# Kernel optimization log

Hardware: AMD Instinct MI355X
Metric: run time of the kernel (lower is better)

## Reference

```python
import jax, jax.numpy as jnp
import numpy as np

B, N, T, D, H, L, N_HOP = 8, 512, 64, 256, 256, 2, 1
NEG = -1e18


def setup_inputs() -> dict:
    key = jax.random.key(0)
    ks = jax.random.split(key, 16)
    sc = 0.05
    return {
        "attn_mem": jax.random.normal(ks[0], (B, N, D), jnp.float32),
        "mem_sizes": jax.random.randint(ks[1], (B,), 1, N + 1).astype(jnp.int32),
        "lstm_in": jax.random.normal(ks[2], (B, T, D), jnp.float32),
        "init_h": jax.random.uniform(ks[3], (L, H), jnp.float32, -0.01, 0.01),
        "init_c": jax.random.uniform(ks[4], (L, H), jnp.float32, -0.01, 0.01),
        "init_i": jax.random.uniform(ks[5], (D,), jnp.float32, -0.1, 0.1),
        # stacked LSTM weights (layer0 input dim D == H so stacking is valid)
        "w_ih": jax.random.normal(ks[6], (L, 4 * H, D), jnp.float32) * sc,
        "w_hh": jax.random.normal(ks[7], (L, 4 * H, H), jnp.float32) * sc,
        "b_ih": jnp.zeros((L, 4 * H), jnp.float32),
        "b_hh": jnp.zeros((L, 4 * H), jnp.float32),
        "attn_wm": jax.random.normal(ks[8], (D, H), jnp.float32) * sc,
        "attn_wq": jax.random.normal(ks[9], (H, H), jnp.float32) * sc,
        "attn_v": jax.random.uniform(ks[10], (H,), jnp.float32, -0.01, 0.01),
        "hop_wm": jax.random.normal(ks[11], (D, H), jnp.float32) * sc,
        "hop_wq": jax.random.normal(ks[12], (H, H), jnp.float32) * sc,
        "hop_v": jax.random.uniform(ks[13], (H,), jnp.float32, -0.01, 0.01),
    }


def _additive_score(feat, query, v, wq):
    # feat: [B,N,H]  query: [B,S,H]  ->  score: [B,S,N]
    q = query @ wq  # [B,S,H]
    s = jnp.tanh(feat[:, None, :, :] + q[:, :, None, :])  # [B,S,N,H] (large)
    return jnp.einsum("bsnh,h->bsn", s, v)


def _run_lstm(x, h0, c0, w_ih, w_hh, b_ih, b_hh):
    # x: [S,B,D] time-major; PyTorch gate order i,f,g,o
    n_layer = h0.shape[0]

    def step(carry, x_t):
        h, c = carry
        inp = x_t
        hs, cs = [], []
        for l in range(n_layer):
            g = inp @ w_ih[l].T + h[l] @ w_hh[l].T + b_ih[l] + b_hh[l]
            i_g, f_g, g_g, o_g = jnp.split(g, 4, axis=-1)
            c_n = jax.nn.sigmoid(f_g) * c[l] + jax.nn.sigmoid(i_g) * jnp.tanh(g_g)
            h_n = jax.nn.sigmoid(o_g) * jnp.tanh(c_n)
            hs.append(h_n)
            cs.append(c_n)
            inp = h_n
        return (jnp.stack(hs), jnp.stack(cs)), inp

    _, ys = jax.lax.scan(step, (h0, c0), x)
    return ys  # [S,B,H]


def reference(attn_mem, mem_sizes, lstm_in, init_h, init_c, init_i,
              w_ih, w_hh, b_ih, b_hh,
              attn_wm, attn_wq, attn_v, hop_wm, hop_wq, hop_v):
    bs, n_mem, _ = attn_mem.shape
    attn_feat = attn_mem @ attn_wm  # [B,N,H]
    hop_feat = attn_mem @ hop_wm    # [B,N,H]

    h0 = jnp.broadcast_to(init_h[:, None, :], (init_h.shape[0], bs, init_h.shape[1]))
    c0 = jnp.broadcast_to(init_c[:, None, :], h0.shape)
    seq = jnp.concatenate(
        [jnp.broadcast_to(init_i[None, None, :], (bs, 1, init_i.shape[0])), lstm_in],
        axis=1,
    )  # [B,T+1,D]
    query = _run_lstm(seq.transpose(1, 0, 2), h0, c0, w_ih, w_hh, b_ih, b_hh)
    query = query.transpose(1, 0, 2)  # [B,T+1,H]

    valid = jnp.arange(n_mem)[None, None, :] < mem_sizes[:, None, None]  # [B,1,N]
    for _ in range(N_HOP):
        score = _additive_score(hop_feat, query, hop_v, hop_wq)  # [B,T+1,N]
        score = jnp.where(valid, score, NEG)
        norm = jax.nn.softmax(score, axis=-1)
        query = jnp.einsum("bsn,bnh->bsh", norm, hop_feat)

    return _additive_score(attn_feat, query, attn_v, attn_wq)  # [B,T+1,N]
```

## Files before the change

### kernel.cpp

```cpp
#include <hip/hip_runtime.h>

#define BB 8
#define NN 512
#define TT 64
#define SS 65
#define DD 256
#define HH 256
#define G4 1024

__device__ __forceinline__ float fsigmoid(float x) {
    return __builtin_amdgcn_rcpf(1.f + __expf(-x));
}
__device__ __forceinline__ float ftanh(float x) {
    float e = __expf(2.f * x);
    return fmaf(-2.f, __builtin_amdgcn_rcpf(e + 1.f), 1.f);
}

__global__ void prep_kernel(const float* __restrict__ lstm_in,
                            const float* __restrict__ init_i,
                            const float* __restrict__ init_h,
                            float* __restrict__ seq,
                            unsigned long long* __restrict__ S0,
                            unsigned long long* __restrict__ S1) {
    int idx = blockIdx.x * 256 + threadIdx.x;
    if (idx < BB * SS * DD) {
        int d = idx & 255;
        int r = idx >> 8;
        int s = r % SS, b = r / SS;
        seq[idx] = (s == 0) ? init_i[d]
                            : lstm_in[((size_t)b * TT + (s - 1)) * DD + d];
    } else {
        int i = idx - BB * SS * DD;
        if (i < 2048) {
            S0[i] = (1ULL << 32) | (unsigned)__float_as_uint(init_h[i & 255]);
        } else if (i < 4096) {
            S1[i - 2048] = (1ULL << 32) | (unsigned)__float_as_uint(init_h[HH + (i & 255)]);
        } else if (i < 4096 + 65 * 2048) {
            S0[2048 + (i - 4096)] = 0ULL;
        } else {
            S1[2048 + (i - (4096 + 65 * 2048))] = 0ULL;
        }
    }
}

__global__ void __launch_bounds__(256) mega_gemm_kernel(
    const float* __restrict__ attn_mem, const float* __restrict__ attn_wm,
    const float* __restrict__ hop_wm, float* __restrict__ attn_feat,
    float* __restrict__ hop_feat, const float* __restrict__ seq,
    const float* __restrict__ w_ih, const float* __restrict__ b_ih,
    const float* __restrict__ b_hh, float* __restrict__ xg0)
{
    __shared__ float As[16][68];
    __shared__ float Bs[16][68];
    __shared__ float Bs2[16][68];
    const int tid = threadIdx.x;
    const int tm = (tid >> 4) * 4, tn = (tid & 15) * 4;
    const int arow = tid >> 2, akq = (tid & 3) << 2;

    if (blockIdx.x < 256) {
        const int bm = (blockIdx.x & 63) * 64, bn = (blockIdx.x >> 6) * 64;
        float acc1[4][4] = {}, acc2[4][4] = {};
        for (int k0 = 0; k0 < 256; k0 += 16) {
            float4 va = *(const float4*)(attn_mem + (size_t)(bm + arow) * 256 + k0 + akq);
            As[akq + 0][arow] = va.x; As[akq + 1][arow] = va.y;
            As[akq + 2][arow] = va.z; As[akq + 3][arow] = va.w;
            int kk = tid >> 4, nq = (tid & 15) << 2;
            *(float4*)&Bs[kk][nq]  = *(const float4*)(attn_wm + (size_t)(k0 + kk) * 256 + bn + nq);
            *(float4*)&Bs2[kk][nq] = *(const float4*)(hop_wm  + (size_t)(k0 + kk) * 256 + bn + nq);
            __syncthreads();
#pragma unroll
            for (int kk2 = 0; kk2 < 16; ++kk2) {
                float4 a  = *(const float4*)&As[kk2][tm];
                float4 b1 = *(const float4*)&Bs[kk2][tn];
                float4 b2 = *(const float4*)&Bs2[kk2][tn];
                float av[4] = {a.x, a.y, a.z, a.w};
                float b1v[4] = {b1.x, b1.y, b1.z, b1.w};
                float b2v[4] = {b2.x, b2.y, b2.z, b2.w};
#pragma unroll
                for (int i = 0; i < 4; ++i)
#pragma unroll
                    for (int jj = 0; jj < 4; ++jj) {
                        acc1[i][jj] = fmaf(av[i], b1v[jj], acc1[i][jj]);
                        acc2[i][jj] = fmaf(av[i], b2v[jj], acc2[i][jj]);
                    }
            }
            __syncthreads();
        }
#pragma unroll
        for (int i = 0; i < 4; ++i) {
            int m = bm + tm + i;
            *(float4*)(attn_feat + (size_t)m * 256 + bn + tn) =
                make_float4(acc1[i][0], acc1[i][1], acc1[i][2], acc1[i][3]);
            *(float4*)(hop_feat + (size_t)m * 256 + bn + tn) =
                make_float4(acc2[i][0], acc2[i][1], acc2[i][2], acc2[i][3]);
        }
    } else {
        const int blk2 = blockIdx.x - 256;
        const int bm = (blk2 % 9) * 64, bn = (blk2 / 9) * 64;
        float acc[4][4] = {};
        for (int k0 = 0; k0 < 256; k0 += 16) {
            {
                int m = bm + arow;
                float4 v = make_float4(0.f, 0.f, 0.f, 0.f);
                if (m < 520) v = *(const float4*)(seq + (size_t)m * 256 + k0 + akq);
                As[akq + 0][arow] = v.x; As[akq + 1][arow] = v.y;
                As[akq + 2][arow] = v.z; As[akq + 3][arow] = v.w;
            }
            {
                int n = bn + arow;
                float4 v = *(const float4*)(w_ih + (size_t)n * 256 + k0 + akq);
                Bs[akq + 0][n - bn] = v.x; Bs[akq + 1][n - bn] = v.y;
                Bs[akq + 2][n - bn] = v.z; Bs[akq + 3][n - bn] = v.w;
            }
            __syncthreads();
#pragma unroll
            for (int kk2 = 0; kk2 < 16; ++kk2) {
                float4 a = *(const float4*)&As[kk2][tm];
                float4 b = *(const float4*)&Bs[kk2][tn];
                float av[4] = {a.x, a.y, a.z, a.w};
                float bv[4] = {b.x, b.y, b.z, b.w};
#pragma unroll
                for (int i = 0; i < 4; ++i)
#pragma unroll
                    for (int jj = 0; jj < 4; ++jj)
                        acc[i][jj] = fmaf(av[i], bv[jj], acc[i][jj]);
            }
            __syncthreads();
        }
        float bad[4];
#pragma unroll
        for (int jj = 0; jj < 4; ++jj)
            bad[jj] = b_ih[bn + tn + jj] + b_hh[bn + tn + jj];
#pragma unroll
        for (int i = 0; i < 4; ++i) {
            int m = bm + tm + i;
            if (m < 520)
                *(float4*)(xg0 + (size_t)m * 1024 + bn + tn) =
                    make_float4(acc[i][0] + bad[0], acc[i][1] + bad[1],
                                acc[i][2] + bad[2], acc[i][3] + bad[3]);
        }
    }
}

__global__ void gemm_kernel(const float* __restrict__ A, const float* __restrict__ B,
                            float* __restrict__ C, int M, int N, int K) {
    __shared__ float As[16][68];
    __shared__ float Bs[16][68];
    const int tid = threadIdx.x;
    const int bm = blockIdx.x * 64, bn = blockIdx.y * 64;
    const int tm = (tid >> 4) * 4, tn = (tid & 15) * 4;
    const int arow = tid >> 2, akq = (tid & 3) << 2;
    float acc[4][4] = {};
    for (int k0 = 0; k0 < K; k0 += 16) {
        {
            int m = bm + arow;
            float4 v = make_float4(0.f, 0.f, 0.f, 0.f);
            if (m < M) v = *(const float4*)(A + (size_t)m * K + k0 + akq);
            As[akq + 0][arow] = v.x; As[akq + 1][arow] = v.y;
            As[akq + 2][arow] = v.z; As[akq + 3][arow] = v.w;
        }
        {
            int kk = tid >> 4, nq = (tid & 15) << 2;
            float4 v = *(const float4*)(B + (size_t)(k0 + kk) * N + bn + nq);
            *(float4*)&Bs[kk][nq] = v;
        }
        __syncthreads();
#pragma unroll
        for (int kk2 = 0; kk2 < 16; ++kk2) {
            float4 a = *(const float4*)&As[kk2][tm];
            float4 b = *(const float4*)&Bs[kk2][tn];
            float av[4] = {a.x, a.y, a.z, a.w};
            float bv[4] = {b.x, b.y, b.z, b.w};
#pragma unroll
            for (int i = 0; i < 4; ++i)
#pragma unroll
                for (int jj = 0; jj < 4; ++jj)
                    acc[i][jj] = fmaf(av[i], bv[jj], acc[i][jj]);
        }
        __syncthreads();
    }
#pragma unroll
    for (int i = 0; i < 4; ++i) {
        int m = bm + tm + i;
        if (m < M)
            *(float4*)(C + (size_t)m * N + bn + tn) =
                make_float4(acc[i][0], acc[i][1], acc[i][2], acc[i][3]);
    }
}

__device__ __forceinline__ float dot16(const float4* w, const float* hp) {
    float4 s = make_float4(0.f, 0.f, 0.f, 0.f);
#pragma unroll
    for (int k = 0; k < 16; ++k) {
        float4 h4 = *(const float4*)(hp + 4 * k);
        s.x = fmaf(w[k].x, h4.x, s.x);
        s.y = fmaf(w[k].y, h4.y, s.y);
        s.z = fmaf(w[k].z, h4.z, s.z);
        s.w = fmaf(w[k].w, h4.w, s.w);
    }
    return (s.x + s.y) + (s.z + s.w);
}

__device__ __forceinline__ float poll_h(const unsigned long long* p, unsigned want) {
    unsigned long long u = __hip_atomic_load(p, __ATOMIC_RELAXED, __HIP_MEMORY_SCOPE_AGENT);
    while ((unsigned)(u >> 32) != want) {
        __builtin_amdgcn_s_sleep(1);
        u = __hip_atomic_load(p, __ATOMIC_RELAXED, __HIP_MEMORY_SCOPE_AGENT);
    }
    return __uint_as_float((unsigned)u);
}

__global__ void __launch_bounds__(1024, 4) lstm_kernel(
    const float* __restrict__ w_ih, const float* __restrict__ w_hh,
    const float* __restrict__ b_ih, const float* __restrict__ b_hh,
    const float* __restrict__ xg0, const float* __restrict__ init_c,
    unsigned long long* __restrict__ S0, unsigned long long* __restrict__ S1,
    float* __restrict__ query)
{
    __shared__ float hls[64 * 68];
    __shared__ float part[1024];
    const int tid = threadIdx.x;
    const int blk = blockIdx.x;
    const int g = tid * 2;
    const int sb = g >> 8, r0 = g & 255, sg0 = r0 >> 6, kq = r0 & 63;
    float* const dst = &hls[(sg0 * 8 + sb) * 68 + kq];

    if (blk < 32) {
        const int jl = tid & 7, gate = (tid >> 3) & 3, b = (tid >> 5) & 7, seg = tid >> 8;
        const int j0 = blk * 8, j = j0 + jl;
        float4 w[16];
        {
            const float4* wr = (const float4*)(w_hh + (size_t)(gate * HH + j) * HH + seg * 64);
#pragma unroll
            for (int k = 0; k < 16; ++k) w[k] = wr[k];
        }
        const int fj = tid >> 3, fb = tid & 7;
        float creg = (tid < 64) ? init_c[j0 + fj] : 0.f;
        const int chunk = seg * 8 + b;
        const int pidx = (chunk * 8 + jl) * 4 + gate;

        for (int t = 0; t < SS; ++t) {
            float xg[4];
            if (tid < 64) {
                const float* xp = xg0 + ((size_t)fb * SS + t) * G4 + (j0 + fj);
#pragma unroll
                for (int gg = 0; gg < 4; ++gg) xg[gg] = xp[gg * 256];
            }
            {
                const unsigned long long* src = S0 + (size_t)t * 2048 + g;
                dst[0] = poll_h(src, (unsigned)(t + 1));
                dst[1] = poll_h(src + 1, (unsigned)(t + 1));
            }
            __syncthreads();
            part[pidx] = dot16(w, &hls[chunk * 68]);
            __syncthreads();
            if (tid < 64) {
                float g0 = xg[0], g1 = xg[1], g2 = xg[2], g3 = xg[3];
#pragma unroll
                for (int s2 = 0; s2 < 4; ++s2) {
                    const float* pp = &part[((s2 * 8 + fb) * 8 + fj) * 4];
                    g0 += pp[0]; g1 += pp[1]; g2 += pp[2]; g3 += pp[3];
                }
                float c = fsigmoid(g1) * creg + fsigmoid(g0) * ftanh(g2);
                float h = fsigmoid(g3) * ftanh(c);
                creg = c;
                unsigned long long u = ((unsigned long long)(unsigned)(t + 2) << 32)
                                     | (unsigned long long)(unsigned)__float_as_uint(h);
                __hip_atomic_store(S0 + (size_t)(t + 1) * 2048 + fb * 256 + (j0 + fj), u,
                                   __ATOMIC_RELAXED, __HIP_MEMORY_SCOPE_AGENT);
            }
        }
    } else {
        const int jl = tid & 3, gate = (tid >> 2) & 3, b = (tid >> 4) & 7, seg = tid >> 7;
        const int j0 = (blk - 32) * 4, j = j0 + jl;
        float4 w[16];
        {
            const float* base = (seg < 4)
                ? (w_ih + (size_t)(G4 + gate * HH + j) * HH + seg * 64)
                : (w_hh + (size_t)(G4 + gate * HH + j) * HH + (seg - 4) * 64);
            const float4* wr = (const float4*)base;
#pragma unroll
            for (int k = 0; k < 16; ++k) w[k] = wr[k];
        }
        const int fj = tid >> 3, fb = tid & 7;
        float creg = 0.f, bias[4] = {0.f, 0.f, 0.f, 0.f};
        if (tid < 32) {
            creg = init_c[HH + j0 + fj];
#pragma unroll
            for (int gg = 0; gg < 4; ++gg)
                bias[gg] = b_ih[G4 + gg * HH + j0 + fj] + b_hh[G4 + gg * HH + j0 + fj];
        }
        const int chunk = seg * 8 + b;
        const int pidx = chunk * 16 + jl * 4 + gate;

        for (int t = 0; t < SS; ++t) {
            {
                const unsigned long long* src = S0 + (size_t)(t + 1) * 2048 + g;
                dst[0] = poll_h(src, (unsigned)(t + 2));
                dst[1] = poll_h(src + 1, (unsigned)(t + 2));
            }
            __syncthreads();
            if (seg < 4) part[pidx] = dot16(w, &hls[chunk * 68]);
            {
                const unsigned long long* src = S1 + (size_t)t * 2048 + g;
                float v0 = poll_h(src, (unsigned)(t + 1));
                float v1 = poll_h(src + 1, (unsigned)(t + 1));
                dst[32 * 68 + 0] = v0;
                dst[32 * 68 + 1] = v1;
            }
            __syncthreads();
            if (seg >= 4) part[pidx] = dot16(w, &hls[chunk * 68]);
            __syncthreads();
            if (tid < 32) {
                float g0 = bias[0], g1 = bias[1], g2 = bias[2], g3 = bias[3];
#pragma unroll
                for (int s2 = 0; s2 < 8; ++s2) {
                    const float* pp = &part[(s2 * 8 + fb) * 16 + fj * 4];
                    g0 += pp[0]; g1 += pp[1]; g2 += pp[2]; g3 += pp[3];
                }
                float c = fsigmoid(g1) * creg + fsigmoid(g0) * ftanh(g2);
                float h = fsigmoid(g3) * ftanh(c);
                creg = c;
                int jj = j0 + fj;
                unsigned long long u = ((unsigned long long)(unsigned)(t + 2) << 32)
                                     | (unsigned long long)(unsigned)__float_as_uint(h);
                __hip_atomic_store(S1 + (size_t)(t + 1) * 2048 + fb * 256 + jj, u,
                                   __ATOMIC_RELAXED, __HIP_MEMORY_SCOPE_AGENT);
                query[((size_t)fb * SS + t) * HH + jj] = h;
            }
        }
    }
}

__global__ void score_kernel(const float* __restrict__ feat, const float* __restrict__ q,
                             const float* __restrict__ v, const int* __restrict__ mem_sizes,
                             float* __restrict__ out, int masked) {
    const int s = blockIdx.x, b = blockIdx.y;
    __shared__ float qs[256], vs[256];
    const int tid = threadIdx.x;
    qs[tid] = q[((size_t)b * SS + s) * HH + tid];
    vs[tid] = v[tid];
    __syncthreads();
    const int lane = tid & 63, wv = tid >> 6;
    const int msize = masked ? mem_sizes[b] : NN;
    const float* fb = feat + (size_t)b * NN * HH + (lane << 2);
    float* ob = out + ((size_t)b * SS + s) * NN;
    for (int n = msize + tid; n < NN; n += 256) ob[n] = -1e18f;
    float4 q4 = *(const float4*)&qs[lane << 2];
    float4 v4 = *(const float4*)&vs[lane << 2];
    int n = wv;
    for (; n + 4 < msize; n += 8) {
        float4 fa = *(const float4*)(fb + (size_t)n * HH);
        float4 fc = *(const float4*)(fb + (size_t)(n + 4) * HH);
        float a0 = ftanh(fa.x + q4.x) * v4.x + ftanh(fa.y + q4.y) * v4.y
                 + ftanh(fa.z + q4.z) * v4.z + ftanh(fa.w + q4.w) * v4.w;
        float a1 = ftanh(fc.x + q4.x) * v4.x + ftanh(fc.y + q4.y) * v4.y
                 + ftanh(fc.z + q4.z) * v4.z + ftanh(fc.w + q4.w) * v4.w;
#pragma unroll
        for (int off = 32; off; off >>= 1) {
            a0 += __shfl_xor(a0, off, 64);
            a1 += __shfl_xor(a1, off, 64);
        }
        if (lane == 0) { ob[n] = a0; ob[n + 4] = a1; }
    }
    for (; n < msize; n += 4) {
        float4 fa = *(const float4*)(fb + (size_t)n * HH);
        float a0 = ftanh(fa.x + q4.x) * v4.x + ftanh(fa.y + q4.y) * v4.y
                 + ftanh(fa.z + q4.z) * v4.z + ftanh(fa.w + q4.w) * v4.w;
#pragma unroll
        for (int off = 32; off; off >>= 1) a0 += __shfl_xor(a0, off, 64);
        if (lane == 0) ob[n] = a0;
    }
}

__global__ void swsum_kernel(const float* __restrict__ score, const float* __restrict__ feat,
                             const int* __restrict__ mem_sizes, float* __restrict__ out) {
    const int b = blockIdx.y, s0 = blockIdx.x * 5;
    const int tid = threadIdx.x;
    __shared__ float ns[5][512];
    for (int i = tid; i < 5 * 512; i += 256)
        ns[i >> 9][i & 511] = score[((size_t)b * SS + s0 + (i >> 9)) * NN + (i & 511)];
    __syncthreads();
    const int wv = tid >> 6, lane = tid & 63;
    for (int r2 = wv; r2 < 5; r2 += 4) {
        float vv[8];
#pragma unroll
        for (int k = 0; k < 8; ++k) vv[k] = ns[r2][lane + 64 * k];
        float m = vv[0];
#pragma unroll
        for (int k = 1; k < 8; ++k) m = fmaxf(m, vv[k]);
#pragma unroll
        for (int off = 32; off; off >>= 1) m = fmaxf(m, __shfl_xor(m, off, 64));
        float l = 0.f;
#pragma unroll
        for (int k = 0; k < 8; ++k) { vv[k] = __expf(vv[k] - m); l += vv[k]; }
#pragma unroll
        for (int off = 32; off; off >>= 1) l += __shfl_xor(l, off, 64);
        float inv = __builtin_amdgcn_rcpf(l);
#pragma unroll
        for (int k = 0; k < 8; ++k) ns[r2][lane + 64 * k] = vv[k] * inv;
    }
    __syncthreads();
    const int msize = mem_sizes[b];
    const int nmax = (msize + 3) & ~3;
    float a0 = 0.f, a1 = 0.f, a2 = 0.f, a3 = 0.f, a4 = 0.f;
    const float* fb = feat + (size_t)b * NN * HH + tid;
    for (int n = 0; n < nmax; n += 4) {
        float f0 = fb[(size_t)(n + 0) * HH];
        float f1 = fb[(size_t)(n + 1) * HH];
        float f2 = fb[(size_t)(n + 2) * HH];
        float f3 = fb[(size_t)(n + 3) * HH];
        a0 += ns[0][n] * f0 + ns[0][n + 1] * f1 + ns[0][n + 2] * f2 + ns[0][n + 3] * f3;
        a1 += ns[1][n] * f0 + ns[1][n + 1] * f1 + ns[1][n + 2] * f2 + ns[1][n + 3] * f3;
        a2 += ns[2][n] * f0 + ns[2][n + 1] * f1 + ns[2][n + 2] * f2 + ns[2][n + 3] * f3;
        a3 += ns[3][n] * f0 + ns[3][n + 1] * f1 + ns[3][n + 2] * f2 + ns[3][n + 3] * f3;
        a4 += ns[4][n] * f0 + ns[4][n + 1] * f1 + ns[4][n + 2] * f2 + ns[4][n + 3] * f3;
    }
    out[((size_t)b * SS + s0 + 0) * HH + tid] = a0;
    out[((size_t)b * SS + s0 + 1) * HH + tid] = a1;
    out[((size_t)b * SS + s0 + 2) * HH + tid] = a2;
    out[((size_t)b * SS + s0 + 3) * HH + tid] = a3;
    out[((size_t)b * SS + s0 + 4) * HH + tid] = a4;
}

extern "C" void kernel_launch(void* const* d_in, const int* in_sizes, int n_in,
                              void* d_out, int out_size, void* d_ws, size_t ws_size,
                              hipStream_t stream) {
    const float* attn_mem  = (const float*)d_in[0];
    const int*   mem_sizes = (const int*)d_in[1];
    const float* lstm_in   = (const float*)d_in[2];
    const float* init_h    = (const float*)d_in[3];
    const float* init_c    = (const float*)d_in[4];
    const float* init_i    = (const float*)d_in[5];
    const float* w_ih      = (const float*)d_in[6];
    const float* w_hh      = (const float*)d_in[7];
    const float* b_ih      = (const float*)d_in[8];
    const float* b_hh      = (const float*)d_in[9];
    const float* attn_wm   = (const float*)d_in[10];
    const float* attn_wq   = (const float*)d_in[11];
    const float* attn_v    = (const float*)d_in[12];
    const float* hop_wm    = (const float*)d_in[13];
    const float* hop_wq    = (const float*)d_in[14];
    const float* hop_v     = (const float*)d_in[15];
    float* out = (float*)d_out;

    float* ws        = (float*)d_ws;
    float* attn_feat = ws;
    float* hop_feat  = ws + 1048576;
    float* seq       = ws + 2097152;
    float* xg0       = ws + 2230272;
    float* query     = ws + 2762752;
    unsigned long long* S0 = (unsigned long long*)(ws + 2895872);
    unsigned long long* S1 = (unsigned long long*)(ws + 3166208);
    float* q1        = ws + 2895872;
    float* score     = ws + 3028992;
    float* query2    = ws + 3295232;
    float* q2        = ws + 3428352;

    prep_kernel<<<1576, 256, 0, stream>>>(lstm_in, init_i, init_h, seq, S0, S1);
    mega_gemm_kernel<<<400, 256, 0, stream>>>(attn_mem, attn_wm, hop_wm, attn_feat,
                                              hop_feat, seq, w_ih, b_ih, b_hh, xg0);
    {
        void* args[] = { (void*)&w_ih, (void*)&w_hh, (void*)&b_ih, (void*)&b_hh,
                         (void*)&xg0, (void*)&init_c, (void*)&S0, (void*)&S1,
                         (void*)&query };
        hipLaunchCooperativeKernel(lstm_kernel, dim3(96), dim3(1024), args, 0u, stream);
    }
    gemm_kernel<<<dim3(9, 4), 256, 0, stream>>>(query, hop_wq, q1, 520, 256, 256);
    score_kernel<<<dim3(65, 8), 256, 0, stream>>>(hop_feat, q1, hop_v, mem_sizes, score, 1);
    swsum_kernel<<<dim3(13, 8), 256, 0, stream>>>(score, hop_feat, mem_sizes, query2);
    gemm_kernel<<<dim3(9, 4), 256, 0, stream>>>(query2, attn_wq, q2, 520, 256, 256);
    score_kernel<<<dim3(65, 8), 256, 0, stream>>>(attn_feat, q2, attn_v, mem_sizes, out, 0);
}
```

Measured before the change: 346.2 us.

## Fuse LSTM with feature GEMMs and collapse post-processing into one kernel

```diff
diff --git a/kernel.cpp b/kernel.cpp
--- a/kernel.cpp
+++ b/kernel.cpp
@@ -16,63 +16,149 @@
     return fmaf(-2.f, __builtin_amdgcn_rcpf(e + 1.f), 1.f);
 }
 
-__global__ void prep_kernel(const float* __restrict__ lstm_in,
-                            const float* __restrict__ init_i,
-                            const float* __restrict__ init_h,
-                            float* __restrict__ seq,
-                            unsigned long long* __restrict__ S0,
-                            unsigned long long* __restrict__ S1) {
-    int idx = blockIdx.x * 256 + threadIdx.x;
-    if (idx < BB * SS * DD) {
-        int d = idx & 255;
-        int r = idx >> 8;
-        int s = r % SS, b = r / SS;
-        seq[idx] = (s == 0) ? init_i[d]
-                            : lstm_in[((size_t)b * TT + (s - 1)) * DD + d];
-    } else {
-        int i = idx - BB * SS * DD;
+__global__ void __launch_bounds__(256) xgprep_kernel(
+    const float* __restrict__ lstm_in, const float* __restrict__ init_i,
+    const float* __restrict__ init_h, const float* __restrict__ w_ih,
+    const float* __restrict__ b_ih, const float* __restrict__ b_hh,
+    float* __restrict__ xg0,
+    unsigned long long* __restrict__ S0, unsigned long long* __restrict__ S1)
+{
+    const int tid = threadIdx.x;
+    if (blockIdx.x >= 144) {
+        int i = (blockIdx.x - 144) * 256 + tid;
         if (i < 2048) {
-            S0[i] = (1ULL << 32) | (unsigned)__float_as_uint(init_h[i & 255]);
+            S0[i] = (1ULL << 32) | (unsigned long long)(unsigned)__float_as_uint(init_h[i & 255]);
         } else if (i < 4096) {
-            S1[i - 2048] = (1ULL << 32) | (unsigned)__float_as_uint(init_h[HH + (i & 255)]);
+            S1[i - 2048] = (1ULL << 32)
+                         | (unsigned long long)(unsigned)__float_as_uint(init_h[HH + (i & 255)]);
         } else if (i < 4096 + 65 * 2048) {
             S0[2048 + (i - 4096)] = 0ULL;
         } else {
             S1[2048 + (i - (4096 + 65 * 2048))] = 0ULL;
         }
-    }
-}
-
-__global__ void __launch_bounds__(256) mega_gemm_kernel(
-    const float* __restrict__ attn_mem, const float* __restrict__ attn_wm,
-    const float* __restrict__ hop_wm, float* __restrict__ attn_feat,
-    float* __restrict__ hop_feat, const float* __restrict__ seq,
-    const float* __restrict__ w_ih, const float* __restrict__ b_ih,
-    const float* __restrict__ b_hh, float* __restrict__ xg0)
-{
+        return;
+    }
     __shared__ float As[16][68];
     __shared__ float Bs[16][68];
-    __shared__ float Bs2[16][68];
-    const int tid = threadIdx.x;
+    const int bm = ((int)blockIdx.x % 9) * 64, bn = ((int)blockIdx.x / 9) * 64;
     const int tm = (tid >> 4) * 4, tn = (tid & 15) * 4;
     const int arow = tid >> 2, akq = (tid & 3) << 2;
-
-    if (blockIdx.x < 256) {
-        const int bm = (blockIdx.x & 63) * 64, bn = (blockIdx.x >> 6) * 64;
+    float acc[4][4] = {};
+    for (int k0 = 0; k0 < 256; k0 += 16) {
+        {
+            int m = bm + arow;
+            float4 v = make_float4(0.f, 0.f, 0.f, 0.f);
+            if (m < 520) {
+                int s = m % 65, b = m / 65;
+                const float* src = (s == 0) ? (init_i + k0 + akq)
+                                            : (lstm_in + ((size_t)b * TT + (s - 1)) * DD + k0 + akq);
+                v = *(const float4*)src;
+            }
+            As[akq + 0][arow] = v.x; As[akq + 1][arow] = v.y;
+            As[akq + 2][arow] = v.z; As[akq + 3][arow] = v.w;
+        }
+        {
+            int n = bn + arow;
+            float4 v = *(const float4*)(w_ih + (size_t)n * 256 + k0 + akq);
+            Bs[akq + 0][n - bn] = v.x; Bs[akq + 1][n - bn] = v.y;
+            Bs[akq + 2][n - bn] = v.z; Bs[akq + 3][n - bn] = v.w;
+        }
+        __syncthreads();
+#pragma unroll
+        for (int kk = 0; kk < 16; ++kk) {
+            float4 a = *(const float4*)&As[kk][tm];
+            float4 b = *(const float4*)&Bs[kk][tn];
+            float av[4] = {a.x, a.y, a.z, a.w};
+            float bv[4] = {b.x, b.y, b.z, b.w};
+#pragma unroll
+            for (int i = 0; i < 4; ++i)
+#pragma unroll
+                for (int jj = 0; jj < 4; ++jj)
+                    acc[i][jj] = fmaf(av[i], bv[jj], acc[i][jj]);
+        }
+        __syncthreads();
+    }
+    float bad[4];
+#pragma unroll
+    for (int jj = 0; jj < 4; ++jj)
+        bad[jj] = b_ih[bn + tn + jj] + b_hh[bn + tn + jj];
+#pragma unroll
+    for (int i = 0; i < 4; ++i) {
+        int m = bm + tm + i;
+        if (m < 520)
+            *(float4*)(xg0 + (size_t)m * 1024 + bn + tn) =
+                make_float4(acc[i][0] + bad[0], acc[i][1] + bad[1],
+                            acc[i][2] + bad[2], acc[i][3] + bad[3]);
+    }
+}
+
+__device__ __forceinline__ float dot16(const float4* w, const float* hp) {
+    float4 s = make_float4(0.f, 0.f, 0.f, 0.f);
+#pragma unroll
+    for (int k = 0; k < 16; ++k) {
+        float4 h4 = *(const float4*)(hp + 4 * k);
+        s.x = fmaf(w[k].x, h4.x, s.x);
+        s.y = fmaf(w[k].y, h4.y, s.y);
+        s.z = fmaf(w[k].z, h4.z, s.z);
+        s.w = fmaf(w[k].w, h4.w, s.w);
+    }
+    return (s.x + s.y) + (s.z + s.w);
+}
+
+__device__ __forceinline__ void poll2(const unsigned long long* p, unsigned want,
+                                      float* d0, float* d1) {
+    unsigned long long a = __hip_atomic_load(p,     __ATOMIC_RELAXED, __HIP_MEMORY_SCOPE_AGENT);
+    unsigned long long b = __hip_atomic_load(p + 1, __ATOMIC_RELAXED, __HIP_MEMORY_SCOPE_AGENT);
+    while ((unsigned)(a >> 32) != want)
+        a = __hip_atomic_load(p, __ATOMIC_RELAXED, __HIP_MEMORY_SCOPE_AGENT);
+    while ((unsigned)(b >> 32) != want)
+        b = __hip_atomic_load(p + 1, __ATOMIC_RELAXED, __HIP_MEMORY_SCOPE_AGENT);
+    *d0 = __uint_as_float((unsigned)a);
+    *d1 = __uint_as_float((unsigned)b);
+}
+
+#define PIN16(w) do { _Pragma("unroll") \
+    for (int _k = 0; _k < 16; ++_k) \
+        asm volatile("" : "+v"(w[_k].x), "+v"(w[_k].y), "+v"(w[_k].z), "+v"(w[_k].w)); \
+} while (0)
+
+__global__ void __launch_bounds__(1024, 4) mega_kernel(
+    const float* __restrict__ w_ih, const float* __restrict__ w_hh,
+    const float* __restrict__ b_ih, const float* __restrict__ b_hh,
+    const float* __restrict__ xg0, const float* __restrict__ init_c,
+    unsigned long long* __restrict__ S0, unsigned long long* __restrict__ S1,
+    float* __restrict__ query,
+    const float* __restrict__ attn_mem, const float* __restrict__ attn_wm,
+    const float* __restrict__ hop_wm,
+    float* __restrict__ attn_feat, float* __restrict__ hop_feat)
+{
+    __shared__ float smem[13056];
+    const int tid = threadIdx.x;
+    const int blk = blockIdx.x;
+
+    if (blk >= 96) {
+        const int grp = tid >> 8, tsub = tid & 255;
+        const int tileid = (blk - 96) * 4 + grp;
+        const int bm = (tileid & 63) * 64, bn = (tileid >> 6) * 64;
+        float* As  = smem + grp * 3264;
+        float* Bs  = As + 1088;
+        float* Bs2 = As + 2176;
+        const int tm = (tsub >> 4) * 4, tn = (tsub & 15) * 4;
+        const int arow = tsub >> 2, akq = (tsub & 3) << 2;
         float acc1[4][4] = {}, acc2[4][4] = {};
         for (int k0 = 0; k0 < 256; k0 += 16) {
             float4 va = *(const float4*)(attn_mem + (size_t)(bm + arow) * 256 + k0 + akq);
-            As[akq + 0][arow] = va.x; As[akq + 1][arow] = va.y;
-            As[akq + 2][arow] = va.z; As[akq + 3][arow] = va.w;
-            int kk = tid >> 4, nq = (tid & 15) << 2;
-            *(float4*)&Bs[kk][nq]  = *(const float4*)(attn_wm + (size_t)(k0 + kk) * 256 + bn + nq);
-            *(float4*)&Bs2[kk][nq] = *(const float4*)(hop_wm  + (size_t)(k0 + kk) * 256 + bn + nq);
+            As[(akq + 0) * 68 + arow] = va.x; As[(akq + 1) * 68 + arow] = va.y;
+            As[(akq + 2) * 68 + arow] = va.z; As[(akq + 3) * 68 + arow] = va.w;
+            int kk = tsub >> 4, nq = (tsub & 15) << 2;
+            *(float4*)&Bs[kk * 68 + nq]  = *(const float4*)(attn_wm + (size_t)(k0 + kk) * 256 + bn + nq);
+            *(float4*)&Bs2[kk * 68 + nq] = *(const float4*)(hop_wm  + (size_t)(k0 + kk) * 256 + bn + nq);
             __syncthreads();
 #pragma unroll
             for (int kk2 = 0; kk2 < 16; ++kk2) {
-                float4 a  = *(const float4*)&As[kk2][tm];
-                float4 b1 = *(const float4*)&Bs[kk2][tn];
-                float4 b2 = *(const float4*)&Bs2[kk2][tn];
+                float4 a  = *(const float4*)&As[kk2 * 68 + tm];
+                float4 b1 = *(const float4*)&Bs[kk2 * 68 + tn];
+                float4 b2 = *(const float4*)&Bs2[kk2 * 68 + tn];
                 float av[4] = {a.x, a.y, a.z, a.w};
                 float b1v[4] = {b1.x, b1.y, b1.z, b1.w};
                 float b2v[4] = {b2.x, b2.y, b2.z, b2.w};
@@ -94,133 +180,11 @@
             *(float4*)(hop_feat + (size_t)m * 256 + bn + tn) =
                 make_float4(acc2[i][0], acc2[i][1], acc2[i][2], acc2[i][3]);
         }
-    } else {
-        const int blk2 = blockIdx.x - 256;
-        const int bm = (blk2 % 9) * 64, bn = (blk2 / 9) * 64;
-        float acc[4][4] = {};
-        for (int k0 = 0; k0 < 256; k0 += 16) {
-            {
-                int m = bm + arow;
-                float4 v = make_float4(0.f, 0.f, 0.f, 0.f);
-                if (m < 520) v = *(const float4*)(seq + (size_t)m * 256 + k0 + akq);
-                As[akq + 0][arow] = v.x; As[akq + 1][arow] = v.y;
-                As[akq + 2][arow] = v.z; As[akq + 3][arow] = v.w;
-            }
-            {
-                int n = bn + arow;
-                float4 v = *(const float4*)(w_ih + (size_t)n * 256 + k0 + akq);
-                Bs[akq + 0][n - bn] = v.x; Bs[akq + 1][n - bn] = v.y;
-                Bs[akq + 2][n - bn] = v.z; Bs[akq + 3][n - bn] = v.w;
-            }
-            __syncthreads();
-#pragma unroll
-            for (int kk2 = 0; kk2 < 16; ++kk2) {
-                float4 a = *(const float4*)&As[kk2][tm];
-                float4 b = *(const float4*)&Bs[kk2][tn];
-                float av[4] = {a.x, a.y, a.z, a.w};
-                float bv[4] = {b.x, b.y, b.z, b.w};
-#pragma unroll
-                for (int i = 0; i < 4; ++i)
-#pragma unroll
-                    for (int jj = 0; jj < 4; ++jj)
-                        acc[i][jj] = fmaf(av[i], bv[jj], acc[i][jj]);
-            }
-            __syncthreads();
-        }
-        float bad[4];
-#pragma unroll
-        for (int jj = 0; jj < 4; ++jj)
-            bad[jj] = b_ih[bn + tn + jj] + b_hh[bn + tn + jj];
-#pragma unroll
-        for (int i = 0; i < 4; ++i) {
-            int m = bm + tm + i;
-            if (m < 520)
-                *(float4*)(xg0 + (size_t)m * 1024 + bn + tn) =
-                    make_float4(acc[i][0] + bad[0], acc[i][1] + bad[1],
-                                acc[i][2] + bad[2], acc[i][3] + bad[3]);
-        }
-    }
-}
-
-__global__ void gemm_kernel(const float* __restrict__ A, const float* __restrict__ B,
-                            float* __restrict__ C, int M, int N, int K) {
-    __shared__ float As[16][68];
-    __shared__ float Bs[16][68];
-    const int tid = threadIdx.x;
-    const int bm = blockIdx.x * 64, bn = blockIdx.y * 64;
-    const int tm = (tid >> 4) * 4, tn = (tid & 15) * 4;
-    const int arow = tid >> 2, akq = (tid & 3) << 2;
-    float acc[4][4] = {};
-    for (int k0 = 0; k0 < K; k0 += 16) {
-        {
-            int m = bm + arow;
-            float4 v = make_float4(0.f, 0.f, 0.f, 0.f);
-            if (m < M) v = *(const float4*)(A + (size_t)m * K + k0 + akq);
-            As[akq + 0][arow] = v.x; As[akq + 1][arow] = v.y;
-            As[akq + 2][arow] = v.z; As[akq + 3][arow] = v.w;
-        }
-        {
-            int kk = tid >> 4, nq = (tid & 15) << 2;
-            float4 v = *(const float4*)(B + (size_t)(k0 + kk) * N + bn + nq);
-            *(float4*)&Bs[kk][nq] = v;
-        }
-        __syncthreads();
-#pragma unroll
-        for (int kk2 = 0; kk2 < 16; ++kk2) {
-            float4 a = *(const float4*)&As[kk2][tm];
-            float4 b = *(const float4*)&Bs[kk2][tn];
-            float av[4] = {a.x, a.y, a.z, a.w};
-            float bv[4] = {b.x, b.y, b.z, b.w};
-#pragma unroll
-            for (int i = 0; i < 4; ++i)
-#pragma unroll
-                for (int jj = 0; jj < 4; ++jj)
-                    acc[i][jj] = fmaf(av[i], bv[jj], acc[i][jj]);
-        }
-        __syncthreads();
-    }
-#pragma unroll
-    for (int i = 0; i < 4; ++i) {
-        int m = bm + tm + i;
-        if (m < M)
-            *(float4*)(C + (size_t)m * N + bn + tn) =
-                make_float4(acc[i][0], acc[i][1], acc[i][2], acc[i][3]);
-    }
-}
-
-__device__ __forceinline__ float dot16(const float4* w, const float* hp) {
-    float4 s = make_float4(0.f, 0.f, 0.f, 0.f);
-#pragma unroll
-    for (int k = 0; k < 16; ++k) {
-        float4 h4 = *(const float4*)(hp + 4 * k);
-        s.x = fmaf(w[k].x, h4.x, s.x);
-        s.y = fmaf(w[k].y, h4.y, s.y);
-        s.z = fmaf(w[k].z, h4.z, s.z);
-        s.w = fmaf(w[k].w, h4.w, s.w);
-    }
-    return (s.x + s.y) + (s.z + s.w);
-}
-
-__device__ __forceinline__ float poll_h(const unsigned long long* p, unsigned want) {
-    unsigned long long u = __hip_atomic_load(p, __ATOMIC_RELAXED, __HIP_MEMORY_SCOPE_AGENT);
-    while ((unsigned)(u >> 32) != want) {
-        __builtin_amdgcn_s_sleep(1);
-        u = __hip_atomic_load(p, __ATOMIC_RELAXED, __HIP_MEMORY_SCOPE_AGENT);
-    }
-    return __uint_as_float((unsigned)u);
-}
-
-__global__ void __launch_bounds__(1024, 4) lstm_kernel(
-    const float* __restrict__ w_ih, const float* __restrict__ w_hh,
-    const float* __restrict__ b_ih, const float* __restrict__ b_hh,
-    const float* __restrict__ xg0, const float* __restrict__ init_c,
-    unsigned long long* __restrict__ S0, unsigned long long* __restrict__ S1,
-    float* __restrict__ query)
-{
-    __shared__ float hls[64 * 68];
-    __shared__ float part[1024];
-    const int tid = threadIdx.x;
-    const int blk = blockIdx.x;
+        return;
+    }
+
+    float* hls  = smem;
+    float* part = smem + 4352;
     const int g = tid * 2;
     const int sb = g >> 8, r0 = g & 255, sg0 = r0 >> 6, kq = r0 & 63;
     float* const dst = &hls[(sg0 * 8 + sb) * 68 + kq];
@@ -234,6 +198,7 @@
 #pragma unroll
             for (int k = 0; k < 16; ++k) w[k] = wr[k];
         }
+        PIN16(w);
         const int fj = tid >> 3, fb = tid & 7;
         float creg = (tid < 64) ? init_c[j0 + fj] : 0.f;
         const int chunk = seg * 8 + b;
@@ -246,11 +211,7 @@
 #pragma unroll
                 for (int gg = 0; gg < 4; ++gg) xg[gg] = xp[gg * 256];
             }
-            {
-                const unsigned long long* src = S0 + (size_t)t * 2048 + g;
-                dst[0] = poll_h(src, (unsigned)(t + 1));
-                dst[1] = poll_h(src + 1, (unsigned)(t + 1));
-            }
+            poll2(S0 + (size_t)t * 2048 + g, (unsigned)(t + 1), &dst[0], &dst[1]);
             __syncthreads();
             part[pidx] = dot16(w, &hls[chunk * 68]);
             __syncthreads();
@@ -282,6 +243,7 @@
 #pragma unroll
             for (int k = 0; k < 16; ++k) w[k] = wr[k];
         }
+        PIN16(w);
         const int fj = tid >> 3, fb = tid & 7;
         float creg = 0.f, bias[4] = {0.f, 0.f, 0.f, 0.f};
         if (tid < 32) {
@@ -294,20 +256,11 @@
         const int pidx = chunk * 16 + jl * 4 + gate;
 
         for (int t = 0; t < SS; ++t) {
-            {
-                const unsigned long long* src = S0 + (size_t)(t + 1) * 2048 + g;
-                dst[0] = poll_h(src, (unsigned)(t + 2));
-                dst[1] = poll_h(src + 1, (unsigned)(t + 2));
-            }
+            poll2(S0 + (size_t)(t + 1) * 2048 + g, (unsigned)(t + 2), &dst[0], &dst[1]);
             __syncthreads();
             if (seg < 4) part[pidx] = dot16(w, &hls[chunk * 68]);
-            {
-                const unsigned long long* src = S1 + (size_t)t * 2048 + g;
-                float v0 = poll_h(src, (unsigned)(t + 1));
-                float v1 = poll_h(src + 1, (unsigned)(t + 1));
-                dst[32 * 68 + 0] = v0;
-                dst[32 * 68 + 1] = v1;
-            }
+            poll2(S1 + (size_t)t * 2048 + g, (unsigned)(t + 1),
+                  &dst[32 * 68], &dst[32 * 68 + 1]);
             __syncthreads();
             if (seg >= 4) part[pidx] = dot16(w, &hls[chunk * 68]);
             __syncthreads();
@@ -332,95 +285,105 @@
     }
 }
 
-__global__ void score_kernel(const float* __restrict__ feat, const float* __restrict__ q,
-                             const float* __restrict__ v, const int* __restrict__ mem_sizes,
-                             float* __restrict__ out, int masked) {
-    const int s = blockIdx.x, b = blockIdx.y;
-    __shared__ float qs[256], vs[256];
-    const int tid = threadIdx.x;
-    qs[tid] = q[((size_t)b * SS + s) * HH + tid];
-    vs[tid] = v[tid];
-    __syncthreads();
+__global__ void __launch_bounds__(256) post_kernel(
+    const float* __restrict__ query, const float* __restrict__ hop_wq,
+    const float* __restrict__ hop_feat, const float* __restrict__ hop_v,
+    const float* __restrict__ attn_wq, const float* __restrict__ attn_feat,
+    const float* __restrict__ attn_v, const int* __restrict__ mem_sizes,
+    float* __restrict__ out)
+{
+    const int s = blockIdx.x, b = blockIdx.y, tid = threadIdx.x;
+    __shared__ float qa[256];
+    __shared__ float qb[256];
+    __shared__ float vv[256];
+    __shared__ float sc[512];
+    __shared__ float red[8];
+    const int msize = mem_sizes[b];
     const int lane = tid & 63, wv = tid >> 6;
-    const int msize = masked ? mem_sizes[b] : NN;
-    const float* fb = feat + (size_t)b * NN * HH + (lane << 2);
-    float* ob = out + ((size_t)b * SS + s) * NN;
-    for (int n = msize + tid; n < NN; n += 256) ob[n] = -1e18f;
-    float4 q4 = *(const float4*)&qs[lane << 2];
-    float4 v4 = *(const float4*)&vs[lane << 2];
-    int n = wv;
-    for (; n + 4 < msize; n += 8) {
-        float4 fa = *(const float4*)(fb + (size_t)n * HH);
-        float4 fc = *(const float4*)(fb + (size_t)(n + 4) * HH);
-        float a0 = ftanh(fa.x + q4.x) * v4.x + ftanh(fa.y + q4.y) * v4.y
-                 + ftanh(fa.z + q4.z) * v4.z + ftanh(fa.w + q4.w) * v4.w;
-        float a1 = ftanh(fc.x + q4.x) * v4.x + ftanh(fc.y + q4.y) * v4.y
-                 + ftanh(fc.z + q4.z) * v4.z + ftanh(fc.w + q4.w) * v4.w;
-#pragma unroll
-        for (int off = 32; off; off >>= 1) {
-            a0 += __shfl_xor(a0, off, 64);
-            a1 += __shfl_xor(a1, off, 64);
-        }
-        if (lane == 0) { ob[n] = a0; ob[n + 4] = a1; }
-    }
-    for (; n < msize; n += 4) {
-        float4 fa = *(const float4*)(fb + (size_t)n * HH);
-        float a0 = ftanh(fa.x + q4.x) * v4.x + ftanh(fa.y + q4.y) * v4.y
-                 + ftanh(fa.z + q4.z) * v4.z + ftanh(fa.w + q4.w) * v4.w;
-#pragma unroll
-        for (int off = 32; off; off >>= 1) a0 += __shfl_xor(a0, off, 64);
-        if (lane == 0) ob[n] = a0;
-    }
-}
-
-__global__ void swsum_kernel(const float* __restrict__ score, const float* __restrict__ feat,
-                             const int* __restrict__ mem_sizes, float* __restrict__ out) {
-    const int b = blockIdx.y, s0 = blockIdx.x * 5;
-    const int tid = threadIdx.x;
-    __shared__ float ns[5][512];
-    for (int i = tid; i < 5 * 512; i += 256)
-        ns[i >> 9][i & 511] = score[((size_t)b * SS + s0 + (i >> 9)) * NN + (i & 511)];
-    __syncthreads();
-    const int wv = tid >> 6, lane = tid & 63;
-    for (int r2 = wv; r2 < 5; r2 += 4) {
-        float vv[8];
-#pragma unroll
-        for (int k = 0; k < 8; ++k) vv[k] = ns[r2][lane + 64 * k];
-        float m = vv[0];
-#pragma unroll
-        for (int k = 1; k < 8; ++k) m = fmaxf(m, vv[k]);
+
+    qa[tid] = query[((size_t)b * SS + s) * HH + tid];
+    vv[tid] = hop_v[tid];
+    __syncthreads();
+    {
+        float a = 0.f;
+        const float* wp = hop_wq + tid;
+#pragma unroll 4
+        for (int h = 0; h < 256; ++h) a = fmaf(qa[h], wp[(size_t)h * 256], a);
+        qb[tid] = a;
+    }
+    __syncthreads();
+    {
+        float4 q4 = *(const float4*)&qb[lane << 2];
+        float4 v4 = *(const float4*)&vv[lane << 2];
+        const float* fb = hop_feat + (size_t)b * NN * HH + (lane << 2);
+        for (int n = wv; n < msize; n += 4) {
+            float4 f4 = *(const float4*)(fb + (size_t)n * HH);
+            float a = ftanh(f4.x + q4.x) * v4.x + ftanh(f4.y + q4.y) * v4.y
+                    + ftanh(f4.z + q4.z) * v4.z + ftanh(f4.w + q4.w) * v4.w;
+#pragma unroll
+            for (int off = 32; off; off >>= 1) a += __shfl_xor(a, off, 64);
+            if (lane == 0) sc[n] = a;
+        }
+    }
+    __syncthreads();
+    {
+        float x0 = (tid < msize) ? sc[tid] : -3e38f;
+        float x1 = (tid + 256 < msize) ? sc[tid + 256] : -3e38f;
+        float m = fmaxf(x0, x1);
 #pragma unroll
         for (int off = 32; off; off >>= 1) m = fmaxf(m, __shfl_xor(m, off, 64));
-        float l = 0.f;
-#pragma unroll
-        for (int k = 0; k < 8; ++k) { vv[k] = __expf(vv[k] - m); l += vv[k]; }
+        if (lane == 0) red[wv] = m;
+        __syncthreads();
+        m = fmaxf(fmaxf(red[0], red[1]), fmaxf(red[2], red[3]));
+        float e0 = __expf(x0 - m), e1 = __expf(x1 - m);
+        float l = e0 + e1;
 #pragma unroll
         for (int off = 32; off; off >>= 1) l += __shfl_xor(l, off, 64);
-        float inv = __builtin_amdgcn_rcpf(l);
-#pragma unroll
-        for (int k = 0; k < 8; ++k) ns[r2][lane + 64 * k] = vv[k] * inv;
-    }
-    __syncthreads();
-    const int msize = mem_sizes[b];
-    const int nmax = (msize + 3) & ~3;
-    float a0 = 0.f, a1 = 0.f, a2 = 0.f, a3 = 0.f, a4 = 0.f;
-    const float* fb = feat + (size_t)b * NN * HH + tid;
-    for (int n = 0; n < nmax; n += 4) {
-        float f0 = fb[(size_t)(n + 0) * HH];
-        float f1 = fb[(size_t)(n + 1) * HH];
-        float f2 = fb[(size_t)(n + 2) * HH];
-        float f3 = fb[(size_t)(n + 3) * HH];
-        a0 += ns[0][n] * f0 + ns[0][n + 1] * f1 + ns[0][n + 2] * f2 + ns[0][n + 3] * f3;
-        a1 += ns[1][n] * f0 + ns[1][n + 1] * f1 + ns[1][n + 2] * f2 + ns[1][n + 3] * f3;
-        a2 += ns[2][n] * f0 + ns[2][n + 1] * f1 + ns[2][n + 2] * f2 + ns[2][n + 3] * f3;
-        a3 += ns[3][n] * f0 + ns[3][n + 1] * f1 + ns[3][n + 2] * f2 + ns[3][n + 3] * f3;
-        a4 += ns[4][n] * f0 + ns[4][n + 1] * f1 + ns[4][n + 2] * f2 + ns[4][n + 3] * f3;
-    }
-    out[((size_t)b * SS + s0 + 0) * HH + tid] = a0;
-    out[((size_t)b * SS + s0 + 1) * HH + tid] = a1;
-    out[((size_t)b * SS + s0 + 2) * HH + tid] = a2;
-    out[((size_t)b * SS + s0 + 3) * HH + tid] = a3;
-    out[((size_t)b * SS + s0 + 4) * HH + tid] = a4;
+        if (lane == 0) red[4 + wv] = l;
+        __syncthreads();
+        float inv = __builtin_amdgcn_rcpf(red[4] + red[5] + red[6] + red[7]);
+        sc[tid] = e0 * inv;
+        sc[tid + 256] = e1 * inv;
+    }
+    __syncthreads();
+    {
+        float a = 0.f;
+        const float* fb = hop_feat + (size_t)b * NN * HH + tid;
+        int n = 0;
+        for (; n + 4 <= msize; n += 4) {
+            a = fmaf(sc[n + 0], fb[(size_t)(n + 0) * HH], a);
+            a = fmaf(sc[n + 1], fb[(size_t)(n + 1) * HH], a);
+            a = fmaf(sc[n + 2], fb[(size_t)(n + 2) * HH], a);
+            a = fmaf(sc[n + 3], fb[(size_t)(n + 3) * HH], a);
+        }
+        for (; n < msize; ++n) a = fmaf(sc[n], fb[(size_t)n * HH], a);
+        __syncthreads();
+        qa[tid] = a;
+    }
+    __syncthreads();
+    {
+        float a = 0.f;
+        const float* wp = attn_wq + tid;
+#pragma unroll 4
+        for (int h = 0; h < 256; ++h) a = fmaf(qa[h], wp[(size_t)h * 256], a);
+        qb[tid] = a;
+        vv[tid] = attn_v[tid];
+    }
+    __syncthreads();
+    {
+        float4 q4 = *(const float4*)&qb[lane << 2];
+        float4 v4 = *(const float4*)&vv[lane << 2];
+        const float* fb = attn_feat + (size_t)b * NN * HH + (lane << 2);
+        float* ob = out + ((size_t)b * SS + s) * NN;
+        for (int n = wv; n < NN; n += 4) {
+            float4 f4 = *(const float4*)(fb + (size_t)n * HH);
+            float a = ftanh(f4.x + q4.x) * v4.x + ftanh(f4.y + q4.y) * v4.y
+                    + ftanh(f4.z + q4.z) * v4.z + ftanh(f4.w + q4.w) * v4.w;
+#pragma unroll
+            for (int off = 32; off; off >>= 1) a += __shfl_xor(a, off, 64);
+            if (lane == 0) ob[n] = a;
+        }
+    }
 }
 
 extern "C" void kernel_launch(void* const* d_in, const int* in_sizes, int n_in,
@@ -447,28 +410,21 @@
     float* ws        = (float*)d_ws;
     float* attn_feat = ws;
     float* hop_feat  = ws + 1048576;
-    float* seq       = ws + 2097152;
-    float* xg0       = ws + 2230272;
-    float* query     = ws + 2762752;
-    unsigned long long* S0 = (unsigned long long*)(ws + 2895872);
-    unsigned long long* S1 = (unsigned long long*)(ws + 3166208);
-    float* q1        = ws + 2895872;
-    float* score     = ws + 3028992;
-    float* query2    = ws + 3295232;
-    float* q2        = ws + 3428352;
-
-    prep_kernel<<<1576, 256, 0, stream>>>(lstm_in, init_i, init_h, seq, S0, S1);
-    mega_gemm_kernel<<<400, 256, 0, stream>>>(attn_mem, attn_wm, hop_wm, attn_feat,
-                                              hop_feat, seq, w_ih, b_ih, b_hh, xg0);
+    float* xg0       = ws + 2097152;
+    float* query     = ws + 2629632;
+    unsigned long long* S0 = (unsigned long long*)(ws + 2762752);
+    unsigned long long* S1 = (unsigned long long*)(ws + 3033088);
+
+    xgprep_kernel<<<1200, 256, 0, stream>>>(lstm_in, init_i, init_h, w_ih,
+                                            b_ih, b_hh, xg0, S0, S1);
     {
         void* args[] = { (void*)&w_ih, (void*)&w_hh, (void*)&b_ih, (void*)&b_hh,
                          (void*)&xg0, (void*)&init_c, (void*)&S0, (void*)&S1,
-                         (void*)&query };
-        hipLaunchCooperativeKernel(lstm_kernel, dim3(96), dim3(1024), args, 0u, stream);
-    }
-    gemm_kernel<<<dim3(9, 4), 256, 0, stream>>>(query, hop_wq, q1, 520, 256, 256);
-    score_kernel<<<dim3(65, 8), 256, 0, stream>>>(hop_feat, q1, hop_v, mem_sizes, score, 1);
-    swsum_kernel<<<dim3(13, 8), 256, 0, stream>>>(score, hop_feat, mem_sizes, query2);
-    gemm_kernel<<<dim3(9, 4), 256, 0, stream>>>(query2, attn_wq, q2, 520, 256, 256);
-    score_kernel<<<dim3(65, 8), 256, 0, stream>>>(attn_feat, q2, attn_v, mem_sizes, out, 0);
-}
+                         (void*)&query, (void*)&attn_mem, (void*)&attn_wm,
+                         (void*)&hop_wm, (void*)&attn_feat, (void*)&hop_feat };
+        hipLaunchCooperativeKernel(mega_kernel, dim3(160), dim3(1024), args, 0u, stream);
+    }
+    post_kernel<<<dim3(65, 8), 256, 0, stream>>>(query, hop_wq, hop_feat, hop_v,
+                                                 attn_wq, attn_feat, attn_v,
+                                                 mem_sizes, out);
+}
```

Result: slower. 354.4 us (+2.4%).
